# Performance work log

Hardware: AMD Instinct MI355X
Metric: run time of the kernel (lower is better)

The kernel has to match this reference:

```python
import jax, jax.numpy as jnp
import numpy as np

jax.config.update("jax_enable_x64", True)  # hash uses int64 (prime * coord ~ 7e12)

FEATURE_DIM = 2
GRID_DIM = 3
NUM_LVL = 16
MAX_RES = 2048
MIN_RES = 16
HASH_POWER = 19
MAX_ENTRY = 2 ** HASH_POWER
PRIMES = (3367900313, 2654435761, 805459861)

_b = np.exp((np.log(MAX_RES) - np.log(MIN_RES)) / (NUM_LVL - 1))
RESOLUTIONS = [int(np.floor(MIN_RES * _b ** i)) for i in range(NUM_LVL)]
TABLE_SIZES = [min(r ** GRID_DIM, MAX_ENTRY) for r in RESOLUTIONS]

# Corner offset order matches get_corner(): [c000, c010, c001, c011, c100, c101, c110, c111]
OFFSETS = np.array([[0, 0, 0], [0, 1, 0], [0, 0, 1], [0, 1, 1],
                    [1, 0, 0], [1, 0, 1], [1, 1, 0], [1, 1, 1]], dtype=np.int64)

N = 1 << 20  # number of query points


def setup_inputs() -> dict:
    key = jax.random.key(0)
    kx, kt = jax.random.split(key)
    x = jax.random.uniform(kx, (N, GRID_DIM), dtype=jnp.float32)  # in [0,1]
    # stacked (padded) hashtables; dense levels only use their first res^3 rows
    tables = jax.random.normal(kt, (NUM_LVL, MAX_ENTRY, FEATURE_DIM), dtype=jnp.float32) * 1e-4
    return {"x": x, "tables": tables}


def _level(x, table, res, table_size):
    resf = float(res)
    coord = jnp.clip(x * (resf - 1.0), 0.0, resf - 1.0001)  # [N,3] hash-space coords
    fl = jnp.floor(coord)
    corners = fl.astype(jnp.int64)[:, None, :] + jnp.asarray(OFFSETS)  # [N,8,3]
    if table_size != MAX_ENTRY:
        # dense spatial index: sum_i c_i * res^i
        idx = corners[..., 0] + corners[..., 1] * res + corners[..., 2] * (res * res)
    else:
        # NGP hash: xor of coord*prime, mod table size
        h = (corners[..., 0] * PRIMES[0]) ^ (corners[..., 1] * PRIMES[1]) ^ (corners[..., 2] * PRIMES[2])
        idx = h % MAX_ENTRY
    feat = table[idx]  # [N,8,F] gather
    d = coord - fl  # fractional part, [N,3]
    xx, yy, zz = d[:, 0], d[:, 1], d[:, 2]
    mx, my, mz = 1.0 - xx, 1.0 - yy, 1.0 - zz
    # weight order matches interpolation_weights() stack order
    w = jnp.stack([mx * my * mz, xx * my * mz, mx * yy * mz, xx * yy * mz,
                   mx * my * zz, xx * my * zz, mx * yy * zz, xx * yy * zz], axis=-1)  # [N,8]
    return (feat * w[..., None]).sum(axis=-2)  # [N,F]


def reference(x, tables):
    outs = [_level(x, tables[l], RESOLUTIONS[l], TABLE_SIZES[l]) for l in range(NUM_LVL)]
    return jnp.concatenate(outs, axis=-1)  # [N, NUM_LVL*FEATURE_DIM]
```

## Files before the change

### kernel.cpp

```cpp
#include <hip/hip_runtime.h>
#include <math.h>

#define NLVL 16
#define MAX_ENTRY (1 << 19)
#define NPTS (1 << 20)

typedef float f2_t __attribute__((ext_vector_type(2)));
typedef float f4_t __attribute__((ext_vector_type(4)));

__device__ __forceinline__ void nt_store4(float4 v, float4* p) {
    f4_t t; t.x = v.x; t.y = v.y; t.z = v.z; t.w = v.w;
    __builtin_nontemporal_store(t, (f4_t*)p);
}
__device__ __forceinline__ void nt_storeu(unsigned v, unsigned* p) {
    __builtin_nontemporal_store(v, p);
}
__device__ __forceinline__ float4 nt_load4(const float4* p) {
    f4_t t = __builtin_nontemporal_load((const f4_t*)p);
    return make_float4(t.x, t.y, t.z, t.w);
}
__device__ __forceinline__ unsigned nt_loadu(const unsigned* p) {
    return __builtin_nontemporal_load(p);
}

__device__ __forceinline__ unsigned pack_bf16(float a, float b) {
    unsigned ua = __float_as_uint(a), ub = __float_as_uint(b);
    ua = (ua + 0x7FFFu + ((ua >> 16) & 1u)) >> 16;
    ub = (ub + 0x7FFFu + ((ub >> 16) & 1u)) >> 16;
    return ua | (ub << 16);
}
__device__ __forceinline__ float bf_lo(unsigned u) { return __uint_as_float(u << 16); }
__device__ __forceinline__ float bf_hi(unsigned u) { return __uint_as_float(u & 0xFFFF0000u); }

__device__ __constant__ int OX[8] = {0, 0, 0, 0, 1, 1, 1, 1};
__device__ __constant__ int OY[8] = {0, 1, 0, 1, 0, 0, 1, 1};
__device__ __constant__ int OZ[8] = {0, 0, 1, 1, 0, 1, 0, 1};

__device__ __forceinline__ void corner_setup(
    float x0, float x1, float x2, float s, float hi,
    int& cx, int& cy, int& cz,
    float (&wx)[2], float (&wy)[2], float (&wz)[2])
{
    float c0 = fminf(fmaxf(x0 * s, 0.0f), hi);
    float c1 = fminf(fmaxf(x1 * s, 0.0f), hi);
    float c2 = fminf(fmaxf(x2 * s, 0.0f), hi);
    float f0 = floorf(c0), f1 = floorf(c1), f2 = floorf(c2);
    cx = (int)f0; cy = (int)f1; cz = (int)f2;
    float xx = c0 - f0, yy = c1 - f1, zz = c2 - f2;
    wx[0] = 1.0f - xx; wx[1] = xx;
    wy[0] = 1.0f - yy; wy[1] = yy;
    wz[0] = 1.0f - zz; wz[1] = zz;
}

__device__ __forceinline__ void acc_pair(
    int j, float4 f, const float (&wx)[2], const float (&wy)[2], const float (&wz)[2],
    float& a0, float& a1)
{
    const float w0 = wx[j & 1] * wy[j >> 1] * wz[0];
    const float w1 = wx[j >> 1] * wy[j & 1] * wz[1];
    a0 += w0 * f.x + w1 * f.z;
    a1 += w0 * f.y + w1 * f.w;
}

struct OptP {
    int   res[NLVL];
    int   res2[NLVL];
    float scale[NLVL];
    float hi[NLVL];
    int   cdim[6];
    long long blkoff[6];
};


__global__ __launch_bounds__(256) void repack3_kernel(
    const float* __restrict__ x,
    const float* __restrict__ tables,
    float4* __restrict__ blk,
    float4* __restrict__ xp,
    OptP P)
{
    const long long stride = (long long)gridDim.x * 256;
    const long long tid = (long long)blockIdx.x * 256 + threadIdx.x;

    for (int l = 0; l < 6; ++l) {
        const int res = P.res[l], res2v = P.res2[l];
        const int cdim = P.cdim[l];
        const long long ncell = (long long)cdim * cdim * cdim;
        const float2* tab = (const float2*)(tables + (size_t)l * MAX_ENTRY * 2);
        float4* dst = blk + P.blkoff[l];
        for (long long c = tid; c < ncell; c += stride) {
            const int cx = (int)(c % cdim);
            const int cy = (int)((c / cdim) % cdim);
            const int cz = (int)(c / ((long long)cdim * cdim));
            const int base = cx + cy * res + cz * res2v;
#pragma unroll
            for (int j = 0; j < 4; ++j) {
                const int oy = j & 1, oz = j >> 1;
                const float2 e0 = tab[base + oy * res + oz * res2v];
                const float2 e1 = tab[base + 1 + oy * res + oz * res2v];
                nt_store4(make_float4(e0.x, e0.y, e1.x, e1.y), &dst[c * 4 + j]);
            }
        }
    }

    for (long long i = tid; i < NPTS; i += stride) {
        xp[i] = make_float4(x[3 * i + 0], x[3 * i + 1], x[3 * i + 2], 0.0f);
    }
}

__global__ __launch_bounds__(256) void mega_kernel(
    const float4* __restrict__ xp,
    const float* __restrict__ tables,
    const float4* __restrict__ blk,
    unsigned* __restrict__ fb,
    OptP P)
{
    const int seg = blockIdx.x >> 11;
    const int lvl = seg + 3;
    const int t = (blockIdx.x & 2047) * 256 + threadIdx.x;
    unsigned* fbl = fb + (size_t)seg * NPTS;

    const float scale = P.scale[lvl], hiv = P.hi[lvl];

#pragma unroll
    for (int h = 0; h < 2; ++h) {
        const int i = t + h * (NPTS / 2);
        const float4 v = nt_load4(&xp[i]);
        int cx, cy, cz;
        float wx[2], wy[2], wz[2];
        corner_setup(v.x, v.y, v.z, scale, hiv, cx, cy, cz, wx, wy, wz);

        float a0 = 0.0f, a1 = 0.0f;

        if (lvl <= 5) {
            const int cdim = P.cdim[lvl];
            const long long c = cx + (long long)cy * cdim + (long long)cz * cdim * cdim;
            const float4* bl = blk + P.blkoff[lvl];
#pragma unroll
            for (int j = 0; j < 4; ++j) {
                const float4 f = bl[c * 4 + j];
                acc_pair(j, f, wx, wy, wz, a0, a1);
            }
        } else {
            const float2* tab = (const float2*)tables + (size_t)lvl * MAX_ENTRY;
            const unsigned P0 = 3367900313u, P1 = 2654435761u, P2 = 805459861u;
            unsigned hx[2], hy[2], hz[2];
            hx[0] = (unsigned)cx * P0; hx[1] = hx[0] + P0;
            hy[0] = (unsigned)cy * P1; hy[1] = hy[0] + P1;
            hz[0] = (unsigned)cz * P2; hz[1] = hz[0] + P2;
#pragma unroll
            for (int k = 0; k < 8; ++k) {
                const unsigned idx = (hx[OX[k]] ^ hy[OY[k]] ^ hz[OZ[k]]) & (MAX_ENTRY - 1);
                const float2 f = tab[idx];
                const float w = wx[k & 1] * wy[(k >> 1) & 1] * wz[k >> 2];
                a0 += w * f.x; a1 += w * f.y;
            }
        }

        nt_storeu(pack_bf16(a0, a1), &fbl[i]);
    }
}

#define ASM_PTS 512
#define ASM_S 513
__global__ __launch_bounds__(256) void assemble2_kernel(
    const float4* __restrict__ xp,
    const float4* __restrict__ blk,
    const unsigned* __restrict__ fb,
    float4* __restrict__ out,
    OptP P)
{
    __shared__ unsigned lds[NLVL * ASM_S];
    const int base = blockIdx.x * ASM_PTS;
    const int tid = threadIdx.x;

#pragma unroll
    for (int s = 3; s < NLVL; ++s) {
        const unsigned* f = fb + (size_t)(s - 3) * NPTS + base;
        lds[s * ASM_S + tid]       = nt_loadu(&f[tid]);
        lds[s * ASM_S + 256 + tid] = nt_loadu(&f[256 + tid]);
    }

#pragma unroll
    for (int h = 0; h < 2; ++h) {
        const int p = tid + h * 256;
        const int i = base + p;
        const float4 v = nt_load4(&xp[i]);
#pragma unroll
        for (int l = 0; l < 3; ++l) {
            int cx, cy, cz;
            float wx[2], wy[2], wz[2];
            corner_setup(v.x, v.y, v.z, P.scale[l], P.hi[l], cx, cy, cz, wx, wy, wz);
            const int cdim = P.cdim[l];
            const long long c = cx + (long long)cy * cdim + (long long)cz * cdim * cdim;
            const float4* bl = blk + P.blkoff[l];
            float a0 = 0.0f, a1 = 0.0f;
#pragma unroll
            for (int j = 0; j < 4; ++j) {
                const float4 f = bl[c * 4 + j];
                acc_pair(j, f, wx, wy, wz, a0, a1);
            }
            lds[l * ASM_S + p] = pack_bf16(a0, a1);
        }
    }

    __syncthreads();

    float4* o4 = out + (size_t)base * 8;
#pragma unroll
    for (int j = 0; j < 16; ++j) {
        const int g = j * 256 + tid;
        const int p = g >> 3;
        const int c = g & 7;
        const unsigned u0 = lds[(2 * c) * ASM_S + p];
        const unsigned u1 = lds[(2 * c + 1) * ASM_S + p];
        nt_store4(make_float4(bf_lo(u0), bf_hi(u0), bf_lo(u1), bf_hi(u1)), &o4[g]);
    }
}


struct DenseParams {
    int   res[6];
    int   res2[6];
    float scale[6];
    float hi[6];
    long long tab_off[6];
};

__device__ __forceinline__ float2 hash_point_fb(
    float x0, float x1, float x2, const float2* __restrict__ tab,
    float scale, float hi)
{
    int cx, cy, cz;
    float wx[2], wy[2], wz[2];
    corner_setup(x0, x1, x2, scale, hi, cx, cy, cz, wx, wy, wz);
    const unsigned P0 = 3367900313u, P1 = 2654435761u, P2 = 805459861u;
    unsigned hx[2], hy[2], hz[2];
    hx[0] = (unsigned)cx * P0; hx[1] = hx[0] + P0;
    hy[0] = (unsigned)cy * P1; hy[1] = hy[0] + P1;
    hz[0] = (unsigned)cz * P2; hz[1] = hz[0] + P2;
    float a0 = 0.0f, a1 = 0.0f;
#pragma unroll
    for (int k = 0; k < 8; ++k) {
        const unsigned idx = (hx[OX[k]] ^ hy[OY[k]] ^ hz[OZ[k]]) & (MAX_ENTRY - 1);
        const float2 f = tab[idx];
        const float w = wx[k & 1] * wy[(k >> 1) & 1] * wz[k >> 2];
        a0 += w * f.x; a1 += w * f.y;
    }
    return make_float2(a0, a1);
}

__global__ __launch_bounds__(256) void dense6_kernel(
    const float* __restrict__ x,
    const float* __restrict__ tables,
    float* __restrict__ out,
    DenseParams P)
{
    const int i = blockIdx.x * 256 + threadIdx.x;
    if (i >= NPTS) return;
    const float x0 = x[3 * i + 0];
    const float x1 = x[3 * i + 1];
    const float x2 = x[3 * i + 2];
    float o[12];
#pragma unroll
    for (int l = 0; l < 6; ++l) {
        int cx, cy, cz;
        float wx[2], wy[2], wz[2];
        corner_setup(x0, x1, x2, P.scale[l], P.hi[l], cx, cy, cz, wx, wy, wz);
        const float2* tab = (const float2*)(tables + P.tab_off[l]);
        const int res  = P.res[l];
        const int res2 = P.res2[l];
        const int base = cx + cy * res + cz * res2;
        float a0 = 0.0f, a1 = 0.0f;
#pragma unroll
        for (int k = 0; k < 8; ++k) {
            const int idx = base + OX[k] + OY[k] * res + OZ[k] * res2;
            const float2 f = tab[idx];
            const float w = wx[k & 1] * wy[(k >> 1) & 1] * wz[k >> 2];
            a0 += w * f.x; a1 += w * f.y;
        }
        o[2 * l + 0] = a0; o[2 * l + 1] = a1;
    }
    float4* op = (float4*)(out + (size_t)i * 32);
    op[0] = ((float4*)o)[0];
    op[1] = ((float4*)o)[1];
    op[2] = ((float4*)o)[2];
}

__global__ __launch_bounds__(256) void hash_level_kernel(
    const float* __restrict__ x,
    const float* __restrict__ tables,
    float* __restrict__ out,
    int level, float scale, float hi)
{
    const int i = blockIdx.x * 256 + threadIdx.x;
    if (i >= NPTS) return;
    const float2* tab = (const float2*)tables + (size_t)level * MAX_ENTRY;
    const float2 r = hash_point_fb(x[3 * i], x[3 * i + 1], x[3 * i + 2], tab, scale, hi);
    *(float2*)(out + (size_t)i * 32 + 2 * level) = r;
}

__global__ __launch_bounds__(256) void generic_level_kernel(
    const float* __restrict__ x,
    const float* __restrict__ tables,
    float* __restrict__ out,
    int level, int res, int res2, int use_hash, float scale, float hi)
{
    const int i = blockIdx.x * 256 + threadIdx.x;
    if (i >= NPTS) return;
    const float x0 = x[3 * i + 0];
    const float x1 = x[3 * i + 1];
    const float x2 = x[3 * i + 2];
    int cx, cy, cz;
    float wx[2], wy[2], wz[2];
    corner_setup(x0, x1, x2, scale, hi, cx, cy, cz, wx, wy, wz);
    const float2* tab = (const float2*)tables + (size_t)level * MAX_ENTRY;
    float a0 = 0.0f, a1 = 0.0f;
    if (use_hash) {
        const unsigned P0 = 3367900313u, P1 = 2654435761u, P2 = 805459861u;
        unsigned hx[2], hy[2], hz[2];
        hx[0] = (unsigned)cx * P0; hx[1] = hx[0] + P0;
        hy[0] = (unsigned)cy * P1; hy[1] = hy[0] + P1;
        hz[0] = (unsigned)cz * P2; hz[1] = hz[0] + P2;
#pragma unroll
        for (int k = 0; k < 8; ++k) {
            const unsigned idx = (hx[OX[k]] ^ hy[OY[k]] ^ hz[OZ[k]]) & (MAX_ENTRY - 1);
            const float2 f = tab[idx];
            const float w = wx[k & 1] * wy[(k >> 1) & 1] * wz[k >> 2];
            a0 += w * f.x; a1 += w * f.y;
        }
    } else {
        const int base = cx + cy * res + cz * res2;
#pragma unroll
        for (int k = 0; k < 8; ++k) {
            const int idx = base + OX[k] + OY[k] * res + OZ[k] * res2;
            const float2 f = tab[idx];
            const float w = wx[k & 1] * wy[(k >> 1) & 1] * wz[k >> 2];
            a0 += w * f.x; a1 += w * f.y;
        }
    }
    *(float2*)(out + (size_t)i * 32 + 2 * level) = make_float2(a0, a1);
}


extern "C" void kernel_launch(void* const* d_in, const int* in_sizes, int n_in,
                              void* d_out, int out_size, void* d_ws, size_t ws_size,
                              hipStream_t stream)
{
    const float* x      = (const float*)d_in[0];
    const float* tables = (const float*)d_in[1];
    float* out          = (float*)d_out;

    int   res[NLVL], res2[NLVL], use_hash[NLVL];
    float scale[NLVL], hi[NLVL];
    const double b = exp((log(2048.0) - log(16.0)) / 15.0);
    for (int l = 0; l < NLVL; ++l) {
        const int r = (int)floor(16.0 * pow(b, (double)l));
        res[l]  = r;
        res2[l] = r * r;
        const long long t3 = (long long)r * r * r;
        use_hash[l] = (t3 >= (long long)MAX_ENTRY) ? 1 : 0;
        scale[l] = (float)(r - 1);
        hi[l]    = (float)((double)r - 1.0001);
    }

    const int block = 256;
    const int grid  = (NPTS + block - 1) / block;

    bool expected = true;
    for (int l = 0; l < 6; ++l)    expected = expected && !use_hash[l];
    for (int l = 6; l < NLVL; ++l) expected = expected && use_hash[l];

    long long blkoff[6];
    long long blkTot = 0;
    for (int l = 0; l < 6; ++l) {
        const long long cd = (long long)res[l] - 1;
        blkoff[l] = blkTot;
        blkTot += cd * cd * cd * 4;
    }
    auto al = [](size_t v) { return (v + 255) & ~(size_t)255; };
    const size_t blkBytes = (size_t)blkTot * 16;
    const size_t offxp = al(blkBytes);
    const size_t offfb = al(offxp + (size_t)NPTS * 16);
    const size_t need  = offfb + (size_t)13 * NPTS * 4;

    if (expected && ws_size >= need) {
        float4* blk  = (float4*)d_ws;
        float4* xp   = (float4*)((char*)d_ws + offxp);
        unsigned* fb = (unsigned*)((char*)d_ws + offfb);

        OptP P;
        for (int l = 0; l < NLVL; ++l) {
            P.res[l] = res[l]; P.res2[l] = res2[l];
            P.scale[l] = scale[l]; P.hi[l] = hi[l];
        }
        for (int l = 0; l < 6; ++l) { P.cdim[l] = res[l] - 1; P.blkoff[l] = blkoff[l]; }

        repack3_kernel<<<2048, block, 0, stream>>>(x, tables, blk, xp, P);
        mega_kernel<<<13 * 2048, block, 0, stream>>>(xp, tables, blk, fb, P);
        assemble2_kernel<<<NPTS / ASM_PTS, block, 0, stream>>>(xp, blk, fb, (float4*)out, P);
    } else if (expected) {
        DenseParams P;
        for (int l = 0; l < 6; ++l) {
            P.res[l] = res[l]; P.res2[l] = res2[l];
            P.scale[l] = scale[l]; P.hi[l] = hi[l];
            P.tab_off[l] = (long long)l * MAX_ENTRY * 2;
        }
        dense6_kernel<<<grid, block, 0, stream>>>(x, tables, out, P);
        for (int l = 6; l < NLVL; ++l) {
            hash_level_kernel<<<grid, block, 0, stream>>>(x, tables, out, l, scale[l], hi[l]);
        }
    } else {
        for (int l = 0; l < NLVL; ++l) {
            generic_level_kernel<<<grid, block, 0, stream>>>(
                x, tables, out, l, res[l], res2[l], use_hash[l], scale[l], hi[l]);
        }
    }
}
```

Baseline: 602.3 us.

## Move coarse dense levels into main kernel, simplify assemble to pure transpose

```diff
diff --git a/kernel.cpp b/kernel.cpp
--- a/kernel.cpp
+++ b/kernel.cpp
@@ -98,7 +98,7 @@
                 const int oy = j & 1, oz = j >> 1;
                 const float2 e0 = tab[base + oy * res + oz * res2v];
                 const float2 e1 = tab[base + 1 + oy * res + oz * res2v];
-                nt_store4(make_float4(e0.x, e0.y, e1.x, e1.y), &dst[c * 4 + j]);
+                dst[c * 4 + j] = make_float4(e0.x, e0.y, e1.x, e1.y);
             }
         }
     }
@@ -115,10 +115,9 @@
     unsigned* __restrict__ fb,
     OptP P)
 {
-    const int seg = blockIdx.x >> 11;
-    const int lvl = seg + 3;
+    const int lvl = blockIdx.x >> 11;
     const int t = (blockIdx.x & 2047) * 256 + threadIdx.x;
-    unsigned* fbl = fb + (size_t)seg * NPTS;
+    unsigned* fbl = fb + (size_t)lvl * NPTS;
 
     const float scale = P.scale[lvl], hiv = P.hi[lvl];
 
@@ -163,47 +162,19 @@
 
 #define ASM_PTS 512
 #define ASM_S 513
-__global__ __launch_bounds__(256) void assemble2_kernel(
-    const float4* __restrict__ xp,
-    const float4* __restrict__ blk,
-    const unsigned* __restrict__ fb,
-    float4* __restrict__ out,
-    OptP P)
+__global__ __launch_bounds__(256) void assemble_t_kernel(
+    const unsigned* __restrict__ fb, float4* __restrict__ out)
 {
     __shared__ unsigned lds[NLVL * ASM_S];
     const int base = blockIdx.x * ASM_PTS;
     const int tid = threadIdx.x;
 
 #pragma unroll
-    for (int s = 3; s < NLVL; ++s) {
-        const unsigned* f = fb + (size_t)(s - 3) * NPTS + base;
+    for (int s = 0; s < NLVL; ++s) {
+        const unsigned* f = fb + (size_t)s * NPTS + base;
         lds[s * ASM_S + tid]       = nt_loadu(&f[tid]);
         lds[s * ASM_S + 256 + tid] = nt_loadu(&f[256 + tid]);
     }
-
-#pragma unroll
-    for (int h = 0; h < 2; ++h) {
-        const int p = tid + h * 256;
-        const int i = base + p;
-        const float4 v = nt_load4(&xp[i]);
-#pragma unroll
-        for (int l = 0; l < 3; ++l) {
-            int cx, cy, cz;
-            float wx[2], wy[2], wz[2];
-            corner_setup(v.x, v.y, v.z, P.scale[l], P.hi[l], cx, cy, cz, wx, wy, wz);
-            const int cdim = P.cdim[l];
-            const long long c = cx + (long long)cy * cdim + (long long)cz * cdim * cdim;
-            const float4* bl = blk + P.blkoff[l];
-            float a0 = 0.0f, a1 = 0.0f;
-#pragma unroll
-            for (int j = 0; j < 4; ++j) {
-                const float4 f = bl[c * 4 + j];
-                acc_pair(j, f, wx, wy, wz, a0, a1);
-            }
-            lds[l * ASM_S + p] = pack_bf16(a0, a1);
-        }
-    }
-
     __syncthreads();
 
     float4* o4 = out + (size_t)base * 8;
@@ -382,7 +353,7 @@
     const size_t blkBytes = (size_t)blkTot * 16;
     const size_t offxp = al(blkBytes);
     const size_t offfb = al(offxp + (size_t)NPTS * 16);
-    const size_t need  = offfb + (size_t)13 * NPTS * 4;
+    const size_t need  = offfb + (size_t)NLVL * NPTS * 4;
 
     if (expected && ws_size >= need) {
         float4* blk  = (float4*)d_ws;
@@ -396,9 +367,9 @@
         }
         for (int l = 0; l < 6; ++l) { P.cdim[l] = res[l] - 1; P.blkoff[l] = blkoff[l]; }
 
-        repack3_kernel<<<2048, block, 0, stream>>>(x, tables, blk, xp, P);
-        mega_kernel<<<13 * 2048, block, 0, stream>>>(xp, tables, blk, fb, P);
-        assemble2_kernel<<<NPTS / ASM_PTS, block, 0, stream>>>(xp, blk, fb, (float4*)out, P);
+        repack3_kernel<<<4096, block, 0, stream>>>(x, tables, blk, xp, P);
+        mega_kernel<<<NLVL * 2048, block, 0, stream>>>(xp, tables, blk, fb, P);
+        assemble_t_kernel<<<NPTS / ASM_PTS, block, 0, stream>>>(fb, (float4*)out);
     } else if (expected) {
         DenseParams P;
         for (int l = 0; l < 6; ++l) {
```

New measurement: 552.4 us. -8.3%, faster.
